# Performance work log

Measured on AMD Instinct MI355X. Metric: run time of the kernel, lower is better.

## Reference

```python
import jax, jax.numpy as jnp
import numpy as np

ALPHA = 1.702
LIMIT = 7.0
TOP_K = 2
B, S, H, E, I = 2, 1024, 768, 8, 768


def setup_inputs() -> dict:
    key = jax.random.key(0)
    ks = jax.random.split(key, 7)
    scale = 0.02
    return {
        "hidden_states": jax.random.normal(ks[0], (B, S, H), dtype=jnp.float32),
        "Wr": jax.random.normal(ks[1], (H, E), dtype=jnp.float32) * scale,
        "br": jax.random.normal(ks[2], (E,), dtype=jnp.float32) * scale,
        "Wgu": jax.random.normal(ks[3], (E, H, 2 * I), dtype=jnp.float32) * scale,
        "bgu": jax.random.normal(ks[4], (E, 2 * I), dtype=jnp.float32) * scale,
        "Wd": jax.random.normal(ks[5], (E, I, H), dtype=jnp.float32) * scale,
        "bd": jax.random.normal(ks[6], (E, H), dtype=jnp.float32) * scale,
    }


def reference(hidden_states, Wr, br, Wgu, bgu, Wd, bd):
    # Router: top-K experts per token, softmax over the K selected logits
    logits = jnp.einsum("bsh,he->bse", hidden_states, Wr) + br
    topk_vals, topk_idx = jax.lax.top_k(logits, TOP_K)        # [B,S,K]
    router_scores = jax.nn.softmax(topk_vals, axis=-1)         # [B,S,K]

    # Dense-over-experts grouped GEMM (sparse_matmul reference: unselected
    # experts are computed but never read by the combine gather below).
    gu = jnp.einsum("bsh,ehf->bsef", hidden_states, Wgu) + bgu  # [B,S,E,2I]
    gu = jnp.minimum(gu, LIMIT)
    gate = gu[..., :I]
    up = jnp.maximum(gu[..., I:], -LIMIT)
    glu = gate * jax.nn.sigmoid(gate * ALPHA)
    activated = (up + 1.0) * glu                                # [B,S,E,I]

    down = jnp.einsum("bsei,eih->bseh", activated, Wd) + bd     # [B,S,E,H]

    # all_to_all_combine (num_devices=1): gather this token's K expert outputs
    sel = jnp.take_along_axis(down, topk_idx[..., None], axis=2)  # [B,S,K,H]
    output = jnp.sum(sel * router_scores[..., None], axis=2)      # [B,S,H]
    return output
```

## Files before the change

kernel.cpp:

```cpp
#include <hip/hip_runtime.h>
#include <hip/hip_bf16.h>
#include <cmath>

#define ALPHA 1.702f
#define LIMIT 7.0f

constexpr int B = 2, S = 1024, H = 768, E = 8, I = 768;
constexpr int T = B * S;
constexpr int TWO_I = 2 * I;
constexpr int CAP = T;
constexpr int NROWS = T * 2;
constexpr int NT1 = I / 64;
constexpr int NT2 = H / 64;
constexpr int MT = CAP / 128;

typedef __attribute__((ext_vector_type(8))) short short8;
typedef __attribute__((ext_vector_type(4))) float floatx4;

__device__ __forceinline__ unsigned short f2bf(float v) {
  __hip_bfloat16 h = __float2bfloat16(v);
  return *reinterpret_cast<unsigned short*>(&h);
}

__device__ __forceinline__ void g2l16(const void* g, void* l) {
  __builtin_amdgcn_global_load_lds(
      (const __attribute__((address_space(1))) void*)g,
      (__attribute__((address_space(3))) void*)l, 16, 0, 0);
}

__global__ __launch_bounds__(64) void router_kernel(
    const float* __restrict__ x, const float* __restrict__ Wr,
    const float* __restrict__ br, int* __restrict__ topk_idx,
    float* __restrict__ topk_w, unsigned short* __restrict__ xb,
    float* __restrict__ out) {
  int t = blockIdx.x;
  int lane = threadIdx.x;
  const float* xr = x + (size_t)t * H;

  float4 z4 = {0.f, 0.f, 0.f, 0.f};
#pragma unroll
  for (int j = 0; j < 3; j++)
    *(float4*)(out + (size_t)t * H + (size_t)(j * 64 + lane) * 4) = z4;

  float acc[E];
#pragma unroll
  for (int e = 0; e < E; e++) acc[e] = 0.0f;

#pragma unroll
  for (int it = 0; it < 3; it++) {
    int h4 = it * 64 + lane;
    float4 xv = *(const float4*)(xr + (size_t)h4 * 4);
    ushort4 xo;
    xo.x = f2bf(xv.x);
    xo.y = f2bf(xv.y);
    xo.z = f2bf(xv.z);
    xo.w = f2bf(xv.w);
    *(ushort4*)(xb + (size_t)t * H + (size_t)h4 * 4) = xo;
    const float* wrow = Wr + (size_t)h4 * 4 * E;
    float xs[4] = {xv.x, xv.y, xv.z, xv.w};
#pragma unroll
    for (int j = 0; j < 4; j++)
#pragma unroll
      for (int e = 0; e < E; e++) acc[e] += xs[j] * wrow[j * E + e];
  }
#pragma unroll
  for (int e = 0; e < E; e++) {
    float v = acc[e];
    for (int off = 32; off > 0; off >>= 1) v += __shfl_down(v, off, 64);
    acc[e] = v;
  }
  if (lane == 0) {
    float logits[E];
#pragma unroll
    for (int e = 0; e < E; e++) logits[e] = acc[e] + br[e];
    int i0 = 0;
    float v0 = logits[0];
#pragma unroll
    for (int e = 1; e < E; e++)
      if (logits[e] > v0) { v0 = logits[e]; i0 = e; }
    int i1 = -1;
    float v1 = -INFINITY;
#pragma unroll
    for (int e = 0; e < E; e++) {
      if (e == i0) continue;
      if (logits[e] > v1) { v1 = logits[e]; i1 = e; }
    }
    float s1 = __expf(v1 - v0);
    float denom = 1.0f + s1;
    topk_idx[t * 2 + 0] = i0;
    topk_idx[t * 2 + 1] = i1;
    topk_w[t * 2 + 0] = 1.0f / denom;
    topk_w[t * 2 + 1] = s1 / denom;
  }
}

__global__ __launch_bounds__(256) void transpose_all(
    const float* __restrict__ Wgu, const float* __restrict__ Wd,
    unsigned short* __restrict__ Wgt, unsigned short* __restrict__ Wdt,
    const int* __restrict__ topk_idx, const float* __restrict__ topk_w,
    int* __restrict__ e_cnt, int* __restrict__ row_token,
    float* __restrict__ row_w) {
  int z = blockIdx.z;
  int tid = threadIdx.x;

  if (z == 16) {
    if (blockIdx.x != 0 || blockIdx.y != 0) return;
    __shared__ int cur[E];
    if (tid < E) cur[tid] = 0;
    __syncthreads();
    for (int i = tid; i < NROWS; i += 256) {
      int e = topk_idx[i];
      int pos = atomicAdd(&cur[e], 1);
      row_token[e * CAP + pos] = i >> 1;
      row_w[e * CAP + pos] = topk_w[i];
    }
    __syncthreads();
    if (tid < E) e_cnt[tid] = cur[tid];
    return;
  }

  int which = z >> 3, e = z & 7;
  int N = which ? H : TWO_I;
  if (which && blockIdx.x >= (H / 64)) return;
  const float* in = which ? (Wd + (size_t)e * H * I)
                          : (Wgu + (size_t)e * H * TWO_I);
  unsigned short* out = which ? (Wdt + (size_t)e * H * I)
                              : (Wgt + (size_t)e * H * TWO_I);
  constexpr int K = 768;
  int n0 = blockIdx.x * 64, k0 = blockIdx.y * 64;

  __shared__ float tile[64][65];
  int jr = tid & 15, r0 = tid >> 4;
#pragma unroll
  for (int p = 0; p < 4; p++) {
    int k = r0 + p * 16;
    float4 v = *(const float4*)(in + (size_t)(k0 + k) * N + n0 + jr * 4);
    tile[k][jr * 4 + 0] = v.x;
    tile[k][jr * 4 + 1] = v.y;
    tile[k][jr * 4 + 2] = v.z;
    tile[k][jr * 4 + 3] = v.w;
  }
  __syncthreads();
#pragma unroll
  for (int p = 0; p < 4; p++) {
    int n = r0 + p * 16;
    ushort4 o;
    o.x = f2bf(tile[jr * 4 + 0][n]);
    o.y = f2bf(tile[jr * 4 + 1][n]);
    o.z = f2bf(tile[jr * 4 + 2][n]);
    o.w = f2bf(tile[jr * 4 + 3][n]);
    *(ushort4*)(out + (size_t)(n0 + n) * K + k0 + jr * 4) = o;
  }
}

__global__ __launch_bounds__(256) void gemm_gu_mfma(
    const unsigned short* __restrict__ xb, const unsigned short* __restrict__ Wgt,
    const float* __restrict__ bgu, const int* __restrict__ e_cnt,
    const int* __restrict__ row_token, unsigned short* __restrict__ act) {
  int bid = blockIdx.x;
  int g = bid % (E * NT1);
  int mt = bid / (E * NT1);
  int e = g / NT1;
  int n0 = (g % NT1) * 64;
  int cnt = e_cnt[e];
  int m0 = mt * 128;
  if (m0 >= cnt) return;
  int start = e * CAP;
  const unsigned short* Wg = Wgt + (size_t)e * TWO_I * H;
  const float* bias = bgu + (size_t)e * TWO_I;

  __shared__ short As[2][128 * 64];
  __shared__ short Bg[2][64 * 64];
  __shared__ short Bu[2][64 * 64];
  __shared__ int tok[128];

  int tid = threadIdx.x;
  if (tid < 128) {
    int m = m0 + tid;
    tok[tid] = row_token[start + ((m < cnt) ? m : (cnt - 1))];
  }
  __syncthreads();

  int lane = tid & 63;
  int wave = tid >> 6;
  int quad = lane >> 4;
  int lrow = lane & 15;
  int wm = (wave >> 1) * 64;
  int wn = (wave & 1) * 32;

  const unsigned short* gA[4];
  int oA[4];
#pragma unroll
  for (int r = 0; r < 4; r++) {
    int s = (wave * 4 + r) * 64 + lane;
    int row = s >> 3;
    int gg = (s & 7) ^ (row & 7);
    gA[r] = xb + (size_t)tok[row] * H + gg * 8;
    oA[r] = (wave * 4 + r) * 64 * 8;
  }
  const unsigned short *gBg[2], *gBu[2];
  int oB[2];
#pragma unroll
  for (int r = 0; r < 2; r++) {
    int s = (wave * 2 + r) * 64 + lane;
    int row = s >> 3;
    int gg = (s & 7) ^ (row & 7);
    gBg[r] = Wg + (size_t)(n0 + row) * H + gg * 8;
    gBu[r] = gBg[r] + (size_t)I * H;
    oB[r] = (wave * 2 + r) * 64 * 8;
  }

  float bgv[2], buv[2];
#pragma unroll
  for (int tj = 0; tj < 2; tj++) {
    int ncol = n0 + wn + tj * 16 + lrow;
    bgv[tj] = bias[ncol];
    buv[tj] = bias[I + ncol];
  }

  floatx4 accg[4][2], accu[4][2];
#pragma unroll
  for (int i = 0; i < 4; i++)
#pragma unroll
    for (int j = 0; j < 2; j++) {
      accg[i][j] = floatx4{0.f, 0.f, 0.f, 0.f};
      accu[i][j] = floatx4{0.f, 0.f, 0.f, 0.f};
    }

  __syncthreads();

#pragma unroll
  for (int r = 0; r < 4; r++) g2l16(gA[r], &As[0][oA[r]]);
#pragma unroll
  for (int r = 0; r < 2; r++) {
    g2l16(gBg[r], &Bg[0][oB[r]]);
    g2l16(gBu[r], &Bu[0][oB[r]]);
  }

  constexpr int NK = H / 64;
  for (int i = 0; i < NK; i++) {
    int cb = i & 1;
    if (i + 1 < NK) {
      int nb = cb ^ 1;
      int k1 = (i + 1) * 64;
#pragma unroll
      for (int r = 0; r < 4; r++) g2l16(gA[r] + k1, &As[nb][oA[r]]);
#pragma unroll
      for (int r = 0; r < 2; r++) {
        g2l16(gBg[r] + k1, &Bg[nb][oB[r]]);
        g2l16(gBu[r] + k1, &Bu[nb][oB[r]]);
      }
      asm volatile("s_waitcnt vmcnt(8)" ::: "memory");
    } else {
      asm volatile("s_waitcnt vmcnt(0)" ::: "memory");
    }
    __builtin_amdgcn_s_barrier();

#pragma unroll
    for (int ks = 0; ks < 2; ks++) {
      int c = ks * 4 + quad;
      short8 a[4], bg[2], bu[2];
#pragma unroll
      for (int ti = 0; ti < 4; ti++) {
        int r = wm + ti * 16 + lrow;
        a[ti] = *(const short8*)(&As[cb][(r * 8 + (c ^ (r & 7))) * 8]);
      }
#pragma unroll
      for (int tj = 0; tj < 2; tj++) {
        int r = wn + tj * 16 + lrow;
        bg[tj] = *(const short8*)(&Bg[cb][(r * 8 + (c ^ (r & 7))) * 8]);
        bu[tj] = *(const short8*)(&Bu[cb][(r * 8 + (c ^ (r & 7))) * 8]);
      }
#pragma unroll
      for (int ti = 0; ti < 4; ti++)
#pragma unroll
        for (int tj = 0; tj < 2; tj++) {
          accg[ti][tj] = __builtin_amdgcn_mfma_f32_16x16x32_bf16(
              a[ti], bg[tj], accg[ti][tj], 0, 0, 0);
          accu[ti][tj] = __builtin_amdgcn_mfma_f32_16x16x32_bf16(
              a[ti], bu[tj], accu[ti][tj], 0, 0, 0);
        }
    }
    __builtin_amdgcn_s_barrier();
  }

#pragma unroll
  for (int ti = 0; ti < 4; ti++) {
#pragma unroll
    for (int tj = 0; tj < 2; tj++) {
      int ncol = n0 + wn + tj * 16 + lrow;
#pragma unroll
      for (int r = 0; r < 4; r++) {
        int m = m0 + wm + ti * 16 + quad * 4 + r;
        if (m < cnt) {
          float gg = accg[ti][tj][r] + bgv[tj];
          float u = accu[ti][tj][r] + buv[tj];
          gg = fminf(gg, LIMIT);
          u = fmaxf(fminf(u, LIMIT), -LIMIT);
          float glu = gg / (1.0f + __expf(-ALPHA * gg));
          act[(size_t)(start + m) * I + ncol] = f2bf((u + 1.0f) * glu);
        }
      }
    }
  }
}

__global__ __launch_bounds__(256) void gemm_down_mfma(
    const unsigned short* __restrict__ act, const unsigned short* __restrict__ Wdt,
    const float* __restrict__ bd, const int* __restrict__ e_cnt,
    const int* __restrict__ row_token, const float* __restrict__ row_w,
    float* __restrict__ out) {
  int bid = blockIdx.x;
  int g = bid % (E * NT2);
  int mt = bid / (E * NT2);
  int e = g / NT2;
  int n0 = (g % NT2) * 64;
  int cnt = e_cnt[e];
  int m0 = mt * 128;
  if (m0 >= cnt) return;
  int start = e * CAP;
  const unsigned short* Wd = Wdt + (size_t)e * H * I;
  const float* bias = bd + (size_t)e * H;

  __shared__ short As[2][128 * 64];
  __shared__ short Bs[2][64 * 64];
  __shared__ int tok[128];
  __shared__ float wts[128];

  int tid = threadIdx.x;
  if (tid < 128) {
    int m = m0 + tid;
    int mm = (m < cnt) ? m : (cnt - 1);
    tok[tid] = row_token[start + mm];
    wts[tid] = row_w[start + mm];
  }
  __syncthreads();

  int lane = tid & 63;
  int wave = tid >> 6;
  int quad = lane >> 4;
  int lrow = lane & 15;
  int wm = (wave >> 1) * 64;
  int wn = (wave & 1) * 32;

  const unsigned short* gA[4];
  int oA[4];
#pragma unroll
  for (int r = 0; r < 4; r++) {
    int s = (wave * 4 + r) * 64 + lane;
    int row = s >> 3;
    int gg = (s & 7) ^ (row & 7);
    int gm = m0 + row;
    int mm = (gm < cnt) ? gm : (cnt - 1);
    gA[r] = act + (size_t)(start + mm) * I + gg * 8;
    oA[r] = (wave * 4 + r) * 64 * 8;
  }
  const unsigned short* gB[2];
  int oB[2];
#pragma unroll
  for (int r = 0; r < 2; r++) {
    int s = (wave * 2 + r) * 64 + lane;
    int row = s >> 3;
    int gg = (s & 7) ^ (row & 7);
    gB[r] = Wd + (size_t)(n0 + row) * I + gg * 8;
    oB[r] = (wave * 2 + r) * 64 * 8;
  }

  float bdv[2];
#pragma unroll
  for (int tj = 0; tj < 2; tj++) bdv[tj] = bias[n0 + wn + tj * 16 + lrow];

  floatx4 acc[4][2];
#pragma unroll
  for (int i = 0; i < 4; i++)
#pragma unroll
    for (int j = 0; j < 2; j++) acc[i][j] = floatx4{0.f, 0.f, 0.f, 0.f};

  __syncthreads();

#pragma unroll
  for (int r = 0; r < 4; r++) g2l16(gA[r], &As[0][oA[r]]);
#pragma unroll
  for (int r = 0; r < 2; r++) g2l16(gB[r], &Bs[0][oB[r]]);

  constexpr int NK = I / 64;
  for (int i = 0; i < NK; i++) {
    int cb = i & 1;
    if (i + 1 < NK) {
      int nb = cb ^ 1;
      int k1 = (i + 1) * 64;
#pragma unroll
      for (int r = 0; r < 4; r++) g2l16(gA[r] + k1, &As[nb][oA[r]]);
#pragma unroll
      for (int r = 0; r < 2; r++) g2l16(gB[r] + k1, &Bs[nb][oB[r]]);
      asm volatile("s_waitcnt vmcnt(6)" ::: "memory");
    } else {
      asm volatile("s_waitcnt vmcnt(0)" ::: "memory");
    }
    __builtin_amdgcn_s_barrier();

#pragma unroll
    for (int ks = 0; ks < 2; ks++) {
      int c = ks * 4 + quad;
      short8 a[4], b[2];
#pragma unroll
      for (int ti = 0; ti < 4; ti++) {
        int r = wm + ti * 16 + lrow;
        a[ti] = *(const short8*)(&As[cb][(r * 8 + (c ^ (r & 7))) * 8]);
      }
#pragma unroll
      for (int tj = 0; tj < 2; tj++) {
        int r = wn + tj * 16 + lrow;
        b[tj] = *(const short8*)(&Bs[cb][(r * 8 + (c ^ (r & 7))) * 8]);
      }
#pragma unroll
      for (int ti = 0; ti < 4; ti++)
#pragma unroll
        for (int tj = 0; tj < 2; tj++)
          acc[ti][tj] = __builtin_amdgcn_mfma_f32_16x16x32_bf16(
              a[ti], b[tj], acc[ti][tj], 0, 0, 0);
    }
    __builtin_amdgcn_s_barrier();
  }

#pragma unroll
  for (int ti = 0; ti < 4; ti++) {
#pragma unroll
    for (int tj = 0; tj < 2; tj++) {
      int ncol = n0 + wn + tj * 16 + lrow;
#pragma unroll
      for (int r = 0; r < 4; r++) {
        int ml = wm + ti * 16 + quad * 4 + r;
        int m = m0 + ml;
        if (m < cnt) {
          atomicAdd(&out[(size_t)tok[ml] * H + ncol],
                    wts[ml] * (acc[ti][tj][r] + bdv[tj]));
        }
      }
    }
  }
}

extern "C" void kernel_launch(void* const* d_in, const int* in_sizes, int n_in,
                              void* d_out, int out_size, void* d_ws,
                              size_t ws_size, hipStream_t stream) {
  const float* x   = (const float*)d_in[0];
  const float* Wr  = (const float*)d_in[1];
  const float* br  = (const float*)d_in[2];
  const float* Wgu = (const float*)d_in[3];
  const float* bgu = (const float*)d_in[4];
  const float* Wd  = (const float*)d_in[5];
  const float* bd  = (const float*)d_in[6];
  float* out = (float*)d_out;

  char* w = (char*)d_ws;
  int* e_cnt = (int*)w;       w += 16 * sizeof(int);
  int* topk_idx = (int*)w;    w += (size_t)T * 2 * sizeof(int);
  float* topk_w = (float*)w;  w += (size_t)T * 2 * sizeof(float);
  int* row_token = (int*)w;   w += (size_t)E * CAP * sizeof(int);
  float* row_w = (float*)w;   w += (size_t)E * CAP * sizeof(float);
  unsigned short* xb  = (unsigned short*)w; w += (size_t)T * H * 2;
  unsigned short* Wgt = (unsigned short*)w; w += (size_t)E * TWO_I * H * 2;
  unsigned short* Wdt = (unsigned short*)w; w += (size_t)E * H * I * 2;
  unsigned short* act = (unsigned short*)w; w += (size_t)E * CAP * I * 2;

  router_kernel<<<T, 64, 0, stream>>>(x, Wr, br, topk_idx, topk_w, xb, out);
  transpose_all<<<dim3(TWO_I / 64, H / 64, 17), 256, 0, stream>>>(
      Wgu, Wd, Wgt, Wdt, topk_idx, topk_w, e_cnt, row_token, row_w);
  gemm_gu_mfma<<<dim3(MT * E * NT1), 256, 0, stream>>>(
      xb, Wgt, bgu, e_cnt, row_token, act);
  gemm_down_mfma<<<dim3(MT * E * NT2), 256, 0, stream>>>(
      act, Wdt, bd, e_cnt, row_token, row_w, out);
}
```

Before: 166.4 us.

## Fuse router, token bucketing and weight transposes into one pre-pass kernel

The separate router kernel and the transpose/bucketing kernel are merged into one launch. Router blocks handle 32 tokens each, bucket their tokens per expert in shared memory, then reserve global slots with one atomic per expert per block, replacing the serial single-block bucketing pass. The weight-transpose tiles run in the same grid, so routing overlaps the transposes. It adds a memset launch for the counters and makes row order within each expert nondeterministic.

```diff
diff --git a/kernel.cpp b/kernel.cpp
--- a/kernel.cpp
+++ b/kernel.cpp
@@ -9,10 +9,14 @@
 constexpr int T = B * S;
 constexpr int TWO_I = 2 * I;
 constexpr int CAP = T;
-constexpr int NROWS = T * 2;
 constexpr int NT1 = I / 64;
 constexpr int NT2 = H / 64;
 constexpr int MT = CAP / 128;
+
+constexpr int RTR_BLKS = 64;
+constexpr int WGU_TILES = E * (TWO_I / 64) * (H / 64);
+constexpr int WD_TILES  = E * (H / 64) * (H / 64);
+constexpr int PRE_BLKS = RTR_BLKS + WGU_TILES + WD_TILES;
 
 typedef __attribute__((ext_vector_type(8))) short short8;
 typedef __attribute__((ext_vector_type(4))) float floatx4;
@@ -28,106 +32,125 @@
       (__attribute__((address_space(3))) void*)l, 16, 0, 0);
 }
 
-__global__ __launch_bounds__(64) void router_kernel(
+__global__ __launch_bounds__(256) void fused_pre(
     const float* __restrict__ x, const float* __restrict__ Wr,
-    const float* __restrict__ br, int* __restrict__ topk_idx,
-    float* __restrict__ topk_w, unsigned short* __restrict__ xb,
-    float* __restrict__ out) {
-  int t = blockIdx.x;
-  int lane = threadIdx.x;
-  const float* xr = x + (size_t)t * H;
-
-  float4 z4 = {0.f, 0.f, 0.f, 0.f};
-#pragma unroll
-  for (int j = 0; j < 3; j++)
-    *(float4*)(out + (size_t)t * H + (size_t)(j * 64 + lane) * 4) = z4;
-
-  float acc[E];
-#pragma unroll
-  for (int e = 0; e < E; e++) acc[e] = 0.0f;
-
-#pragma unroll
-  for (int it = 0; it < 3; it++) {
-    int h4 = it * 64 + lane;
-    float4 xv = *(const float4*)(xr + (size_t)h4 * 4);
-    ushort4 xo;
-    xo.x = f2bf(xv.x);
-    xo.y = f2bf(xv.y);
-    xo.z = f2bf(xv.z);
-    xo.w = f2bf(xv.w);
-    *(ushort4*)(xb + (size_t)t * H + (size_t)h4 * 4) = xo;
-    const float* wrow = Wr + (size_t)h4 * 4 * E;
-    float xs[4] = {xv.x, xv.y, xv.z, xv.w};
-#pragma unroll
-    for (int j = 0; j < 4; j++)
-#pragma unroll
-      for (int e = 0; e < E; e++) acc[e] += xs[j] * wrow[j * E + e];
-  }
-#pragma unroll
-  for (int e = 0; e < E; e++) {
-    float v = acc[e];
-    for (int off = 32; off > 0; off >>= 1) v += __shfl_down(v, off, 64);
-    acc[e] = v;
-  }
-  if (lane == 0) {
-    float logits[E];
-#pragma unroll
-    for (int e = 0; e < E; e++) logits[e] = acc[e] + br[e];
-    int i0 = 0;
-    float v0 = logits[0];
-#pragma unroll
-    for (int e = 1; e < E; e++)
-      if (logits[e] > v0) { v0 = logits[e]; i0 = e; }
-    int i1 = -1;
-    float v1 = -INFINITY;
+    const float* __restrict__ br, const float* __restrict__ Wgu,
+    const float* __restrict__ Wd, unsigned short* __restrict__ Wgt,
+    unsigned short* __restrict__ Wdt, unsigned short* __restrict__ xb,
+    float* __restrict__ out, int* __restrict__ e_cnt,
+    int* __restrict__ row_token, float* __restrict__ row_w) {
+  int bid = blockIdx.x;
+  int tid = threadIdx.x;
+
+  if (bid < RTR_BLKS) {
+    __shared__ int cnt_s[E];
+    __shared__ int base_s[E];
+    __shared__ int tok_e[E][64];
+    __shared__ float wv_e[E][64];
+
+    if (tid < E) cnt_s[tid] = 0;
+    __syncthreads();
+
+    int wave = tid >> 6;
+    int lane = tid & 63;
+
+    for (int tt = 0; tt < 8; tt++) {
+      int t = bid * 32 + wave * 8 + tt;
+      const float* xr = x + (size_t)t * H;
+
+      float4 z4 = {0.f, 0.f, 0.f, 0.f};
+#pragma unroll
+      for (int j = 0; j < 3; j++)
+        *(float4*)(out + (size_t)t * H + (size_t)(j * 64 + lane) * 4) = z4;
+
+      float acc[E];
+#pragma unroll
+      for (int e = 0; e < E; e++) acc[e] = 0.0f;
+
+#pragma unroll
+      for (int it = 0; it < 3; it++) {
+        int h4 = it * 64 + lane;
+        float4 xv = *(const float4*)(xr + (size_t)h4 * 4);
+        ushort4 xo;
+        xo.x = f2bf(xv.x);
+        xo.y = f2bf(xv.y);
+        xo.z = f2bf(xv.z);
+        xo.w = f2bf(xv.w);
+        *(ushort4*)(xb + (size_t)t * H + (size_t)h4 * 4) = xo;
+        const float* wrow = Wr + (size_t)h4 * 4 * E;
+        float xs[4] = {xv.x, xv.y, xv.z, xv.w};
+#pragma unroll
+        for (int j = 0; j < 4; j++)
+#pragma unroll
+          for (int e = 0; e < E; e++) acc[e] += xs[j] * wrow[j * E + e];
+      }
+#pragma unroll
+      for (int e = 0; e < E; e++) {
+        float v = acc[e];
+        for (int off = 32; off > 0; off >>= 1) v += __shfl_down(v, off, 64);
+        acc[e] = v;
+      }
+      if (lane == 0) {
+        float logits[E];
+#pragma unroll
+        for (int e = 0; e < E; e++) logits[e] = acc[e] + br[e];
+        int i0 = 0;
+        float v0 = logits[0];
+#pragma unroll
+        for (int e = 1; e < E; e++)
+          if (logits[e] > v0) { v0 = logits[e]; i0 = e; }
+        int i1 = -1;
+        float v1 = -INFINITY;
+#pragma unroll
+        for (int e = 0; e < E; e++) {
+          if (e == i0) continue;
+          if (logits[e] > v1) { v1 = logits[e]; i1 = e; }
+        }
+        float s1 = __expf(v1 - v0);
+        float denom = 1.0f + s1;
+        int p0 = atomicAdd(&cnt_s[i0], 1);
+        tok_e[i0][p0] = t;
+        wv_e[i0][p0] = 1.0f / denom;
+        int p1 = atomicAdd(&cnt_s[i1], 1);
+        tok_e[i1][p1] = t;
+        wv_e[i1][p1] = s1 / denom;
+      }
+    }
+    __syncthreads();
+    if (tid < E) base_s[tid] = atomicAdd(&e_cnt[tid], cnt_s[tid]);
+    __syncthreads();
 #pragma unroll
     for (int e = 0; e < E; e++) {
-      if (e == i0) continue;
-      if (logits[e] > v1) { v1 = logits[e]; i1 = e; }
-    }
-    float s1 = __expf(v1 - v0);
-    float denom = 1.0f + s1;
-    topk_idx[t * 2 + 0] = i0;
-    topk_idx[t * 2 + 1] = i1;
-    topk_w[t * 2 + 0] = 1.0f / denom;
-    topk_w[t * 2 + 1] = s1 / denom;
-  }
-}
-
-__global__ __launch_bounds__(256) void transpose_all(
-    const float* __restrict__ Wgu, const float* __restrict__ Wd,
-    unsigned short* __restrict__ Wgt, unsigned short* __restrict__ Wdt,
-    const int* __restrict__ topk_idx, const float* __restrict__ topk_w,
-    int* __restrict__ e_cnt, int* __restrict__ row_token,
-    float* __restrict__ row_w) {
-  int z = blockIdx.z;
-  int tid = threadIdx.x;
-
-  if (z == 16) {
-    if (blockIdx.x != 0 || blockIdx.y != 0) return;
-    __shared__ int cur[E];
-    if (tid < E) cur[tid] = 0;
-    __syncthreads();
-    for (int i = tid; i < NROWS; i += 256) {
-      int e = topk_idx[i];
-      int pos = atomicAdd(&cur[e], 1);
-      row_token[e * CAP + pos] = i >> 1;
-      row_w[e * CAP + pos] = topk_w[i];
-    }
-    __syncthreads();
-    if (tid < E) e_cnt[tid] = cur[tid];
+      int c = cnt_s[e], b0 = base_s[e];
+      for (int j = tid; j < c; j += 256) {
+        row_token[e * CAP + b0 + j] = tok_e[e][j];
+        row_w[e * CAP + b0 + j] = wv_e[e][j];
+      }
+    }
     return;
   }
 
-  int which = z >> 3, e = z & 7;
-  int N = which ? H : TWO_I;
-  if (which && blockIdx.x >= (H / 64)) return;
-  const float* in = which ? (Wd + (size_t)e * H * I)
-                          : (Wgu + (size_t)e * H * TWO_I);
-  unsigned short* out = which ? (Wdt + (size_t)e * H * I)
-                              : (Wgt + (size_t)e * H * TWO_I);
+  int q = bid - RTR_BLKS;
+  const float* in;
+  unsigned short* outw;
+  int N, n0, k0;
+  if (q < WGU_TILES) {
+    int e = q / 288, rem = q % 288;
+    N = TWO_I;
+    n0 = (rem % 24) * 64;
+    k0 = (rem / 24) * 64;
+    in = Wgu + (size_t)e * H * TWO_I;
+    outw = Wgt + (size_t)e * TWO_I * H;
+  } else {
+    int q2 = q - WGU_TILES;
+    int e = q2 / 144, rem = q2 % 144;
+    N = H;
+    n0 = (rem % 12) * 64;
+    k0 = (rem / 12) * 64;
+    in = Wd + (size_t)e * H * I;
+    outw = Wdt + (size_t)e * H * I;
+  }
   constexpr int K = 768;
-  int n0 = blockIdx.x * 64, k0 = blockIdx.y * 64;
 
   __shared__ float tile[64][65];
   int jr = tid & 15, r0 = tid >> 4;
@@ -149,7 +172,7 @@
     o.y = f2bf(tile[jr * 4 + 1][n]);
     o.z = f2bf(tile[jr * 4 + 2][n]);
     o.w = f2bf(tile[jr * 4 + 3][n]);
-    *(ushort4*)(out + (size_t)(n0 + n) * K + k0 + jr * 4) = o;
+    *(ushort4*)(outw + (size_t)(n0 + n) * K + k0 + jr * 4) = o;
   }
 }
 
@@ -455,8 +478,6 @@
 
   char* w = (char*)d_ws;
   int* e_cnt = (int*)w;       w += 16 * sizeof(int);
-  int* topk_idx = (int*)w;    w += (size_t)T * 2 * sizeof(int);
-  float* topk_w = (float*)w;  w += (size_t)T * 2 * sizeof(float);
   int* row_token = (int*)w;   w += (size_t)E * CAP * sizeof(int);
   float* row_w = (float*)w;   w += (size_t)E * CAP * sizeof(float);
   unsigned short* xb  = (unsigned short*)w; w += (size_t)T * H * 2;
@@ -464,9 +485,9 @@
   unsigned short* Wdt = (unsigned short*)w; w += (size_t)E * H * I * 2;
   unsigned short* act = (unsigned short*)w; w += (size_t)E * CAP * I * 2;
 
-  router_kernel<<<T, 64, 0, stream>>>(x, Wr, br, topk_idx, topk_w, xb, out);
-  transpose_all<<<dim3(TWO_I / 64, H / 64, 17), 256, 0, stream>>>(
-      Wgu, Wd, Wgt, Wdt, topk_idx, topk_w, e_cnt, row_token, row_w);
+  hipMemsetAsync(e_cnt, 0, 16 * sizeof(int), stream);
+  fused_pre<<<PRE_BLKS, 256, 0, stream>>>(
+      x, Wr, br, Wgu, Wd, Wgt, Wdt, xb, out, e_cnt, row_token, row_w);
   gemm_gu_mfma<<<dim3(MT * E * NT1), 256, 0, stream>>>(
       xb, Wgt, bgu, e_cnt, row_token, act);
   gemm_down_mfma<<<dim3(MT * E * NT2), 256, 0, stream>>>(
```

Result: no change. 163.8 us (-1.6%).
